# Performance work log

Hardware: AMD Instinct MI355X
Metric: run time of the kernel (lower is better)

Reference implementation:

```python
import jax, jax.numpy as jnp
import numpy as np
from jax import lax

B, C, H, W = 2, 64, 192, 192
KS = 3
N = KS * KS
L = 3  # num_gdns (ResBlocks)


def conv2d(x, w, b=None, padding=0):
    out = lax.conv_general_dilated(x, w, (1, 1), [(padding, padding)] * 2,
                                   dimension_numbers=('NCHW', 'OIHW', 'NCHW'))
    if b is not None:
        out = out + b[None, :, None, None]
    return out


def gdn(x, beta, gamma):
    # y = x / sqrt(beta + sum_j gamma_ij x_j^2)  (inverse=False)
    norm = conv2d(x * x, gamma[:, :, None, None], beta)
    return x / jnp.sqrt(norm)


def resblock(x, w1, w2, beta, gamma):
    res = x
    h = jax.nn.celu(gdn(conv2d(x, w1, padding=0), beta, gamma))  # conv1: no pad (H-2)
    return conv2d(h, w2, padding=2) + res  # conv2: pad 2 restores H


def deform_conv(x, offset, w_dc):
    # DCNv1 (pure-pytorch impl): offset (b,2N,h,w), rows first then cols.
    b, c, Hh, Ww = x.shape
    h, w = offset.shape[2], offset.shape[3]
    pad = 1
    xp = jnp.pad(x, ((0, 0), (0, 0), (pad, pad), (pad, pad)))
    Hp, Wp = Hh + 2 * pad, Ww + 2 * pad
    r = (KS - 1) // 2
    knr, knc = jnp.meshgrid(jnp.arange(-r, r + 1), jnp.arange(-r, r + 1), indexing='ij')
    p_n = jnp.concatenate([knr.reshape(-1), knc.reshape(-1)]).astype(x.dtype)  # (2N,)
    gr, gc = jnp.meshgrid(jnp.arange(1, h + 1), jnp.arange(1, w + 1), indexing='ij')
    p0 = jnp.concatenate([jnp.broadcast_to(gr[None], (N, h, w)),
                          jnp.broadcast_to(gc[None], (N, h, w))], 0).astype(x.dtype)  # (2N,h,w)
    p = p0[None] + p_n[None, :, None, None] + offset  # (b,2N,h,w)
    p = jnp.transpose(p, (0, 2, 3, 1))  # (b,h,w,2N)
    pr = jnp.clip(p[..., :N], 0, Hp - 1)
    pc = jnp.clip(p[..., N:], 0, Wp - 1)
    q0 = lax.stop_gradient(jnp.floor(p))
    qr0 = jnp.clip(q0[..., :N], 0, Hp - 1).astype(jnp.int32)
    qc0 = jnp.clip(q0[..., N:], 0, Wp - 1).astype(jnp.int32)
    qr1 = jnp.clip(q0[..., :N] + 1, 0, Hp - 1).astype(jnp.int32)
    qc1 = jnp.clip(q0[..., N:] + 1, 0, Wp - 1).astype(jnp.int32)
    # bilinear weights (match torch impl exactly)
    g_lt = (1 + (qr0 - pr)) * (1 + (qc0 - pc))
    g_rb = (1 - (qr1 - pr)) * (1 - (qc1 - pc))
    g_lb = (1 + (qr0 - pr)) * (1 - (qc1 - pc))
    g_rt = (1 - (qr1 - pr)) * (1 + (qc0 - pc))
    xf = xp.reshape(b, c, Hp * Wp)

    def gather(qr, qc):
        idx = (qr * Wp + qc).reshape(b, -1)  # (b, h*w*N)
        g = jax.vmap(lambda xb, ib: xb[:, ib])(xf, idx)  # (b,c,h*w*N)
        return g.reshape(b, c, h, w, N)

    xo = (g_lt[:, None] * gather(qr0, qc0) + g_rb[:, None] * gather(qr1, qc1)
          + g_lb[:, None] * gather(qr0, qc1) + g_rt[:, None] * gather(qr1, qc0))
    # stride-ks conv over reshaped x_offset == contraction over (c, n)
    wf = w_dc.reshape(w_dc.shape[0], c, N)
    return jnp.einsum('bchwn,ocn->bohw', xo, wf)


def setup_inputs() -> dict:
    key = jax.random.key(0)
    ks = jax.random.split(key, 11)
    f_r = jax.random.normal(ks[0], (B, C, H, W), jnp.float32)
    m_t = jax.random.normal(ks[1], (B, C, H, W), jnp.float32)
    w_pconv = jax.random.normal(ks[2], (2 * N, C, KS, KS), jnp.float32) * 0.01
    b_pconv = jax.random.normal(ks[3], (2 * N,), jnp.float32) * 0.01
    w_dc = jax.random.normal(ks[4], (C, C, KS, KS), jnp.float32) * 0.05
    w_cat = jax.random.normal(ks[5], (C, 2 * C, KS, KS), jnp.float32) * 0.05
    b_cat = jax.random.normal(ks[6], (C,), jnp.float32) * 0.05
    rb_w1 = jax.random.normal(ks[7], (L, C, C, KS, KS), jnp.float32) * 0.01
    rb_w2 = jax.random.normal(ks[8], (L, C, C, KS, KS), jnp.float32) * 0.01
    rb_beta = jax.random.uniform(ks[9], (L, C), jnp.float32) * 0.5 + 0.5
    rb_gamma = jnp.broadcast_to(0.1 * jnp.eye(C, dtype=jnp.float32), (L, C, C)) \
        + jax.random.uniform(ks[10], (L, C, C), jnp.float32) * 0.01
    return {"f_r": f_r, "m_t": m_t, "w_pconv": w_pconv, "b_pconv": b_pconv,
            "w_dc": w_dc, "w_cat": w_cat, "b_cat": b_cat,
            "rb_w1": rb_w1, "rb_w2": rb_w2, "rb_beta": rb_beta, "rb_gamma": rb_gamma}


def reference(f_r, m_t, w_pconv, b_pconv, w_dc, w_cat, b_cat, rb_w1, rb_w2, rb_beta, rb_gamma):
    offset = conv2d(m_t, w_pconv, b_pconv, padding=1)  # (B, 2N, H, W)
    x = deform_conv(f_r, offset, w_dc)                  # (B, C, H, W)
    y = conv2d(jnp.concatenate([x, f_r], axis=1), w_cat, b_cat, padding=1)
    for i in range(L):
        y = resblock(y, rb_w1[i], rb_w2[i], rb_beta[i], rb_gamma[i])
    return y + x
```

## Files before the change

kernel.cpp:

```cpp
#include <hip/hip_runtime.h>

typedef __attribute__((ext_vector_type(8))) __bf16 bf16x8;
typedef __attribute__((ext_vector_type(4))) __bf16 bf16x4;
typedef __attribute__((ext_vector_type(16))) float f32x16;
typedef __attribute__((ext_vector_type(4))) float f32x4;
typedef __attribute__((ext_vector_type(4))) int i32x4;

#define HH 192
#define WW 192
#define HW 36864
#define HW1 36100

#define TCS 144
#define RP66 (66 * TCS)
#define GDNPITCH 144
#define TREG 8704
#define TROW 5120
#define NPREP 1417

__device__ inline f32x16 mfma32(bf16x8 a, bf16x8 b, f32x16 c) {
  return __builtin_amdgcn_mfma_f32_32x32x16_bf16(a, b, c, 0, 0, 0);
}

__device__ inline f32x16 zero16() {
  f32x16 z;
#pragma unroll
  for (int e = 0; e < 16; ++e) z[e] = 0.f;
  return z;
}

__global__ __launch_bounds__(256) void prep_and_nhwc(
    const float* __restrict__ wp, const float* __restrict__ bp,
    const float* __restrict__ wdc, const float* __restrict__ wcat,
    const float* __restrict__ w1, const float* __restrict__ w2,
    const float* __restrict__ gamma,
    __bf16* __restrict__ wpA, __bf16* __restrict__ wdcA,
    __bf16* __restrict__ wcatA, __bf16* __restrict__ w1A,
    __bf16* __restrict__ w2A, __bf16* __restrict__ gA,
    float* __restrict__ bpad,
    const float* __restrict__ fr, const float* __restrict__ mt,
    __bf16* __restrict__ frn, __bf16* __restrict__ mtn) {
  __shared__ __align__(16) __bf16 tile[64 * 72];
  if (blockIdx.x >= NPREP) {
    int rem2 = blockIdx.x - NPREP;
    int tensor = rem2 / 1152, rem = rem2 % 1152;
    int b = rem / 576, p0 = (rem % 576) * 64;
    const float* src = (tensor ? mt : fr) + (size_t)b * 64 * HW;
    __bf16* dst = (tensor ? mtn : frn) + (size_t)b * HW * 64;
    int tid = threadIdx.x, c = tid >> 2, q0 = (tid & 3) * 16;
    const float* sp = src + (size_t)c * HW + p0 + q0;
#pragma unroll
    for (int qq = 0; qq < 4; ++qq) {
      f32x4 v = *(const f32x4*)(sp + qq * 4);
#pragma unroll
      for (int e = 0; e < 4; ++e) tile[(q0 + qq * 4 + e) * 72 + c] = (__bf16)v[e];
    }
    __syncthreads();
    int px = tid >> 2, c0 = (tid & 3) * 16;
    bf16x8 a = *(const bf16x8*)(&tile[px * 72 + c0]);
    bf16x8 b8 = *(const bf16x8*)(&tile[px * 72 + c0 + 8]);
    __bf16* dp = dst + (size_t)(p0 + px) * 64 + c0;
    *(bf16x8*)dp = a;
    *(bf16x8*)(dp + 8) = b8;
    return;
  }
  int i = blockIdx.x * 256 + threadIdx.x;
  if (i < 18432) {
    int j = i & 7, lane = (i >> 3) & 63, kc = (i >> 9) & 3, n = i >> 11;
    int o = lane & 31, c = kc * 16 + ((lane >> 5) << 3) + j;
    wpA[i] = (o < 18) ? (__bf16)wp[(o * 64 + c) * 9 + n] : (__bf16)0.f;
    return;
  }
  i -= 18432;
  if (i < 36864) {
    int j = i & 7, lane = (i >> 3) & 63, ot = (i >> 9) & 1, kc = (i >> 10) & 3, n = i >> 12;
    int o = ot * 32 + (lane & 31), c = kc * 16 + ((lane >> 5) << 3) + j;
    wdcA[i] = (__bf16)wdc[(o * 64 + c) * 9 + n];
    return;
  }
  i -= 36864;
  if (i < 73728) {
    int d = i, j = d & 7; d >>= 3; int lane = d & 63; d >>= 6; int ot = d & 1; d >>= 1;
    int kc = d & 7; int n = d >> 3;
    int o = ot * 32 + (lane & 31), c = kc * 16 + ((lane >> 5) << 3) + j;
    wcatA[i] = (__bf16)wcat[(o * 128 + c) * 9 + n];
    return;
  }
  i -= 73728;
  if (i < 110592) {
    int l = i / 36864, di = i % 36864, d = di;
    int j = d & 7; d >>= 3; int lane = d & 63; d >>= 6; int ot = d & 1; d >>= 1;
    int kc = d & 3; int n = d >> 2;
    int o = ot * 32 + (lane & 31), c = kc * 16 + ((lane >> 5) << 3) + j;
    w1A[l * 36864 + di] = (__bf16)w1[l * 36864 + (o * 64 + c) * 9 + n];
    return;
  }
  i -= 110592;
  if (i < 110592) {
    int l = i / 36864, di = i % 36864, d = di;
    int j = d & 7; d >>= 3; int lane = d & 63; d >>= 6; int ot = d & 1; d >>= 1;
    int kc = d & 3; int n = d >> 2;
    int o = ot * 32 + (lane & 31), c = kc * 16 + ((lane >> 5) << 3) + j;
    w2A[l * 36864 + di] = (__bf16)w2[l * 36864 + (o * 64 + c) * 9 + n];
    return;
  }
  i -= 110592;
  if (i < 12288) {
    int l = i / 4096, di = i % 4096, d = di;
    int j = d & 7; d >>= 3; int lane = d & 63; d >>= 6; int ot = d & 1; d >>= 1;
    int kc = d & 3;
    int o = ot * 32 + (lane & 31), c = kc * 16 + ((lane >> 5) << 3) + j;
    gA[l * 4096 + di] = (__bf16)gamma[l * 4096 + o * 64 + c];
    return;
  }
  i -= 12288;
  if (i < 96) bpad[i] = (i < 18) ? bp[i] : 0.f;
}

template <int ROWS, int COLS, int TPB>
__device__ inline void stage_bf16T(const __bf16* __restrict__ src,
                                   int srcH, int srcW, int row0, int col0,
                                   unsigned char* lds) {
  for (int i = threadIdx.x; i < ROWS * COLS * 8; i += TPB) {
    int r = i / (COLS * 8), rem = i - r * (COLS * 8), j = rem >> 3, u = rem & 7;
    int gr = row0 + r, gc = col0 + j;
    bf16x8 v;
#pragma unroll
    for (int e = 0; e < 8; ++e) v[e] = (__bf16)0.f;
    if (gr >= 0 && gr < srcH && gc >= 0 && gc < srcW)
      v = *(const bf16x8*)(src + ((size_t)gr * srcW + gc) * 64 + u * 8);
    *(bf16x8*)(lds + r * (COLS * TCS) + j * TCS + u * 16) = v;
  }
}

__device__ inline void stage_glds(const __bf16* __restrict__ src, int H, int W,
                                  int gr, int gc0, const __bf16* __restrict__ zpad,
                                  unsigned char* ldsrow, int chunk) {
  int l = threadIdx.x & 63;
  int colg = l >> 3, gsrc = (l & 7) ^ colg;
  int gc = gc0 + chunk * 8 + colg;
  const __bf16* gp = zpad;
  if (gr >= 0 && gr < H && gc >= 0 && gc < W)
    gp = src + ((size_t)gr * W + gc) * 64 + gsrc * 8;
  __builtin_amdgcn_global_load_lds(
      (const __attribute__((address_space(1))) void*)gp,
      (__attribute__((address_space(3))) void*)(ldsrow + chunk * 1024), 16, 0, 0);
}

template <int KCW>
__device__ inline void tapG1(const __bf16* __restrict__ aB, int ot, int pt,
                             const unsigned char* __restrict__ tile,
                             int n, int koff, f32x16& acc) {
  int lane = threadIdx.x & 63;
  int m = lane & 31, half = lane >> 5;
  int kh = n / 3, kw = n % 3;
  int p = kw + m, p7 = p & 7;
  bf16x8 A[4], B[4];
#pragma unroll
  for (int kc = 0; kc < 4; ++kc)
    A[kc] = *(const bf16x8*)(aB + (size_t)((n * KCW + koff + kc) * 2 + ot) * 512);
#pragma unroll
  for (int kc = 0; kc < 4; ++kc) {
    int gsl = ((kc * 2 + half) ^ p7) << 4;
    B[kc] = *(const bf16x8*)(tile + (kh + pt) * TROW + p * 128 + gsl);
  }
#pragma unroll
  for (int kc = 0; kc < 4; ++kc) acc = mfma32(A[kc], B[kc], acc);
}

__device__ inline void treg_write(const f32x16& a, int ot, unsigned char* reg) {
  int lane = threadIdx.x & 63;
  int m = lane & 31, half = lane >> 5;
#pragma unroll
  for (int g = 0; g < 4; ++g) {
    int o = ot * 32 + half * 4 + g * 8;
    f32x4 v;
    v[0] = a[g * 4 + 0]; v[1] = a[g * 4 + 1];
    v[2] = a[g * 4 + 2]; v[3] = a[g * 4 + 3];
    *(f32x4*)(reg + (m * 68 + o) * 4) = v;
  }
}

__device__ inline void merge_write(const f32x16 acc[2], unsigned char* mb) {
  int l = threadIdx.x & 63;
  unsigned char* p = mb + l * 128;
#pragma unroll
  for (int pt = 0; pt < 2; ++pt)
#pragma unroll
    for (int i = 0; i < 4; ++i) {
      f32x4 v;
      v[0] = acc[pt][i * 4 + 0]; v[1] = acc[pt][i * 4 + 1];
      v[2] = acc[pt][i * 4 + 2]; v[3] = acc[pt][i * 4 + 3];
      *(f32x4*)(p + (((pt * 4 + i) ^ (l & 7)) * 16)) = v;
    }
}
__device__ inline void merge_add(f32x16 acc[2], const unsigned char* mb) {
  int l = threadIdx.x & 63;
  const unsigned char* p = mb + l * 128;
#pragma unroll
  for (int pt = 0; pt < 2; ++pt)
#pragma unroll
    for (int i = 0; i < 4; ++i) {
      f32x4 v = *(const f32x4*)(p + (((pt * 4 + i) ^ (l & 7)) * 16));
      acc[pt][i * 4 + 0] += v[0]; acc[pt][i * 4 + 1] += v[1];
      acc[pt][i * 4 + 2] += v[2]; acc[pt][i * 4 + 3] += v[3];
    }
}

__device__ inline void acc32_to_lds(const f32x16 acc[2], unsigned char* reg) {
  int lane = threadIdx.x & 63;
  int colb = lane & 31, half = lane >> 5;
#pragma unroll
  for (int ot = 0; ot < 2; ++ot)
#pragma unroll
    for (int g = 0; g < 4; ++g) {
      int o = ot * 32 + half * 4 + g * 8;
      f32x4 v;
      v[0] = acc[ot][g * 4 + 0]; v[1] = acc[ot][g * 4 + 1];
      v[2] = acc[ot][g * 4 + 2]; v[3] = acc[ot][g * 4 + 3];
      *(f32x4*)(reg + (colb * 68 + o) * 4) = v;
    }
}

__global__ __launch_bounds__(256, 1) void pconv_mfma(
    const __bf16* __restrict__ mtn, const __bf16* __restrict__ wpA,
    const float* __restrict__ bpad, float* __restrict__ off20) {
  __shared__ __align__(16) unsigned char smem[6 * RP66];
  int b = blockIdx.x / 144, r = blockIdx.x % 144, rt = r / 3, ct = r % 3;
  int h0 = rt * 4, w0 = ct * 64;
  int wid = threadIdx.x >> 6, lane = threadIdx.x & 63;
  int colb = lane & 31, half = lane >> 5, kh8 = half << 3;
  stage_bf16T<6, 66, 256>(mtn + (size_t)b * HW * 64, 192, 192, h0 - 1, w0 - 1, smem);
  const __bf16* aB = wpA + lane * 8;
  bf16x8 pcur[4], pnxt[4];
#pragma unroll
  for (int kc = 0; kc < 4; ++kc) pcur[kc] = *(const bf16x8*)(aB + kc * 512);
  __syncthreads();
  f32x16 acc[2];
  acc[0] = zero16(); acc[1] = zero16();
  {
    const unsigned char* bB = smem + wid * RP66 + colb * TCS + kh8 * 2;
#pragma unroll
    for (int n = 0; n < 9; ++n) {
      if (n < 8) {
#pragma unroll
        for (int kc = 0; kc < 4; ++kc)
          pnxt[kc] = *(const bf16x8*)(aB + ((n + 1) * 4 + kc) * 512);
      }
      const int kh = n / 3, kw = n % 3;
#pragma unroll
      for (int kc = 0; kc < 4; ++kc) {
        const unsigned char* bp = bB + kh * RP66 + kw * TCS + kc * 32;
        bf16x8 b0 = *(const bf16x8*)(bp);
        bf16x8 b1 = *(const bf16x8*)(bp + 32 * TCS);
        acc[0] = mfma32(pcur[kc], b0, acc[0]);
        acc[1] = mfma32(pcur[kc], b1, acc[1]);
      }
#pragma unroll
      for (int kc = 0; kc < 4; ++kc) pcur[kc] = pnxt[kc];
    }
  }
  __syncthreads();
  unsigned char* reg = smem + wid * 9216;
#pragma unroll
  for (int pt = 0; pt < 2; ++pt)
#pragma unroll
    for (int g = 0; g < 4; ++g) {
      int o = half * 4 + g * 8;
      f32x4 v;
      v[0] = acc[pt][g * 4 + 0]; v[1] = acc[pt][g * 4 + 1];
      v[2] = acc[pt][g * 4 + 2]; v[3] = acc[pt][g * 4 + 3];
      *(f32x4*)(reg + ((pt * 32 + colb) * 36 + o) * 4) = v;
    }
  __builtin_amdgcn_s_waitcnt(0);
  size_t pix = (size_t)b * HW + (size_t)(h0 + wid) * 192 + w0 + lane;
#pragma unroll
  for (int q = 0; q < 5; ++q) {
    f32x4 v = *(const f32x4*)(reg + (lane * 36 + q * 4) * 4);
    v += *(const f32x4*)(bpad + q * 4);
    *(f32x4*)(off20 + pix * 20 + q * 4) = v;
  }
}

#define GOPITCH 32
#define DTBL (9 * 32 * GOPITCH)
#define DBUF 4608
#define DLDS (DTBL + 4 * DBUF)
__global__ __launch_bounds__(256, 2) void deform_mfma(
    const __bf16* __restrict__ frn, const float* __restrict__ off20,
    const __bf16* __restrict__ wdcA, float* __restrict__ xlow,
    __bf16* __restrict__ xlowb) {
  __shared__ __align__(16) unsigned char smem[DLDS];
  int bid = (blockIdx.x & 7) * 288 + (blockIdx.x >> 3);
  int b = bid / 1152, r = bid % 1152;
  int h = r / 6, s = r % 6;
  int w0 = s * 32;
  int tid = threadIdx.x;
  int wid = tid >> 6, lane = tid & 63;
  int m = lane & 31, half = lane >> 5;
  int pxg = lane >> 3, slot = lane & 7;
  const __bf16* xb = frn + (size_t)b * HW * 64;
  {
    int px = tid & 31, g = tid >> 5;
    int w = w0 + px;
    size_t pixl = (size_t)b * HW + (size_t)h * 192 + w;
    const float* ofp = off20 + pixl * 20;
    for (int n = g; n < 9; n += 8) {
      float offr = ofp[n], offc = ofp[9 + n];
      float pr = (float)(h + 1 + n / 3 - 1) + offr;
      float pc = (float)(w + 1 + n % 3 - 1) + offc;
      float prc = fminf(fmaxf(pr, 0.f), 193.f);
      float pcc = fminf(fmaxf(pc, 0.f), 193.f);
      float f0r = floorf(pr), f0c = floorf(pc);
      int qr0 = (int)fminf(fmaxf(f0r, 0.f), 193.f);
      int qc0 = (int)fminf(fmaxf(f0c, 0.f), 193.f);
      int qr1 = (int)fminf(fmaxf(f0r + 1.f, 0.f), 193.f);
      int qc1 = (int)fminf(fmaxf(f0c + 1.f, 0.f), 193.f);
      float dr0 = 1.f + ((float)qr0 - prc);
      float dr1 = 1.f - ((float)qr1 - prc);
      float dc0 = 1.f + ((float)qc0 - pcc);
      float dc1 = 1.f - ((float)qc1 - pcc);
      int o0, o1, o2, o3; float g0, g1, g2, g3;
      { bool v = (qr0 >= 1 && qr0 <= 192 && qc0 >= 1 && qc0 <= 192);
        o0 = min(max(qr0-1,0),191)*WW + min(max(qc0-1,0),191); g0 = v ? dr0*dc0 : 0.f; }
      { bool v = (qr1 >= 1 && qr1 <= 192 && qc1 >= 1 && qc1 <= 192);
        o1 = min(max(qr1-1,0),191)*WW + min(max(qc1-1,0),191); g1 = v ? dr1*dc1 : 0.f; }
      { bool v = (qr0 >= 1 && qr0 <= 192 && qc1 >= 1 && qc1 <= 192);
        o2 = min(max(qr0-1,0),191)*WW + min(max(qc1-1,0),191); g2 = v ? dr0*dc1 : 0.f; }
      { bool v = (qr1 >= 1 && qr1 <= 192 && qc0 >= 1 && qc0 <= 192);
        o3 = min(max(qr1-1,0),191)*WW + min(max(qc0-1,0),191); g3 = v ? dr1*dc0 : 0.f; }
      unsigned char* dst = smem + (n * 32 + px) * GOPITCH;
      f32x4 gv; gv[0] = g0; gv[1] = g1; gv[2] = g2; gv[3] = g3;
      i32x4 ov; ov[0] = o0; ov[1] = o1; ov[2] = o2; ov[3] = o3;
      *(f32x4*)dst = gv;
      *(i32x4*)(dst + 16) = ov;
    }
  }
  __syncthreads();
  f32x16 acc[2];
  acc[0] = zero16(); acc[1] = zero16();
  const __bf16* aB = wdcA + lane * 8;
  unsigned char* buf = smem + DTBL + wid * DBUF;
  const unsigned char* bB = buf + m * TCS + (half << 3) * 2;
  int n0 = (wid == 0) ? 0 : (wid * 2 + 1);
  int nn = (wid == 0) ? 3 : 2;

  bf16x8 C[4][4];
  f32x4 G[4];
  bf16x8 a[8];

  auto load_tap = [&](int n) {
#pragma unroll
    for (int i = 0; i < 4; ++i) {
      const unsigned char* gp = smem + (size_t)(n * 32 + i * 8 + pxg) * GOPITCH;
      i32x4 oi = *(const i32x4*)(gp + 16);
      G[i] = *(const f32x4*)gp;
#pragma unroll
      for (int j = 0; j < 4; ++j)
        C[i][j] = *(const bf16x8*)(xb + (size_t)oi[j] * 64 + slot * 8);
    }
  };
  auto load_a = [&](int n) {
#pragma unroll
    for (int kc = 0; kc < 4; ++kc) {
      a[kc * 2 + 0] = *(const bf16x8*)(aB + ((n * 4 + kc) * 2 + 0) * 512);
      a[kc * 2 + 1] = *(const bf16x8*)(aB + ((n * 4 + kc) * 2 + 1) * 512);
    }
  };
  auto blend_write = [&]() {
#pragma unroll
    for (int i = 0; i < 4; ++i) {
      bf16x8 ov;
#pragma unroll
      for (int e = 0; e < 8; ++e) {
        float f = G[i][0] * (float)C[i][0][e] + G[i][1] * (float)C[i][1][e] +
                  G[i][2] * (float)C[i][2][e] + G[i][3] * (float)C[i][3][e];
        ov[e] = (__bf16)f;
      }
      *(bf16x8*)(buf + (i * 8 + pxg) * TCS + slot * 16) = ov;
    }
  };
  auto consume = [&]() {
#pragma unroll
    for (int kc = 0; kc < 4; ++kc) {
      bf16x8 b0 = *(const bf16x8*)(bB + kc * 32);
      acc[0] = mfma32(a[kc * 2 + 0], b0, acc[0]);
      acc[1] = mfma32(a[kc * 2 + 1], b0, acc[1]);
    }
  };

  load_tap(n0);
  blend_write();
  for (int t = 1; t < nn; ++t) {
    load_a(n0 + t - 1);
    load_tap(n0 + t);
    consume();
    asm volatile("s_waitcnt lgkmcnt(0)" ::: "memory");
    blend_write();
  }
  load_a(n0 + nn - 1);
  consume();
  __syncthreads();
  if (wid) merge_write(acc, smem + (wid - 1) * 8192);
  __syncthreads();
  if (wid == 0) {
    merge_add(acc, smem);
    merge_add(acc, smem + 8192);
    merge_add(acc, smem + 16384);
    __builtin_amdgcn_s_waitcnt(0);
    unsigned char* reg = smem;
    acc32_to_lds(acc, reg);
    __builtin_amdgcn_s_waitcnt(0);
    int colb = m, ch = half * 32;
    size_t pix = (size_t)b * HW + (size_t)h * 192 + w0 + colb;
    float* dp = xlow + pix * 64 + ch;
    __bf16* dpb = xlowb + pix * 64 + ch;
#pragma unroll
    for (int q = 0; q < 8; ++q) {
      f32x4 v = *(const f32x4*)(reg + (colb * 68 + ch + q * 4) * 4);
      *(f32x4*)(dp + q * 4) = v;
      bf16x4 o8;
#pragma unroll
      for (int e = 0; e < 4; ++e) o8[e] = (__bf16)v[e];
      *(bf16x4*)(dpb + q * 4) = o8;
    }
  }
}

__global__ __launch_bounds__(256, 4) void convcat_mfma(
    const __bf16* __restrict__ xlowb, const __bf16* __restrict__ frn,
    const __bf16* __restrict__ wA, const float* __restrict__ bias,
    const __bf16* __restrict__ zpad, __bf16* __restrict__ y) {
  __shared__ __align__(16) unsigned char smem[2 * 4 * TROW];
  int bid = (blockIdx.x & 7) * 144 + (blockIdx.x >> 3);
  int b = bid / 576, r = bid % 576, rt = r / 6, ct = r % 6;
  int h0 = rt * 2, w0 = ct * 32;
  int tid = threadIdx.x, wid = tid >> 6, lane = tid & 63;
  int pt = wid & 1, ot = wid >> 1;
  int m = lane & 31, half = lane >> 5;
  const __bf16* src0 = xlowb + (size_t)b * HW * 64;
  const __bf16* src1 = frn + (size_t)b * HW * 64;
  for (int o = wid; o < 40; o += 4) {
    int t = o / 20, rr = (o % 20) / 5, ck = o % 5;
    stage_glds(t ? src1 : src0, 192, 192, h0 - 1 + rr, w0 - 1, zpad,
               smem + t * (4 * TROW) + rr * TROW, ck);
  }
  __syncthreads();
  const __bf16* aB = wA + lane * 8;
  f32x16 acc = zero16();
#pragma unroll
  for (int n = 0; n < 9; ++n) tapG1<8>(aB, ot, pt, smem, n, 0, acc);
#pragma unroll
  for (int n = 0; n < 9; ++n) tapG1<8>(aB, ot, pt, smem + 4 * TROW, n, 4, acc);
  __syncthreads();
  treg_write(acc, ot, smem + pt * TREG);
  __syncthreads();
  {
    const unsigned char* reg = smem + pt * TREG;
    int ch = ot * 32 + half * 16;
    int row = h0 + pt;
    __bf16* dp = y + ((size_t)b * HW + (size_t)row * 192 + w0 + m) * 64 + ch;
#pragma unroll
    for (int q = 0; q < 4; ++q) {
      f32x4 v = *(const f32x4*)(reg + (m * 68 + ch + q * 4) * 4);
      v += *(const f32x4*)(bias + ch + q * 4);
      bf16x4 o8;
#pragma unroll
      for (int e = 0; e < 4; ++e) o8[e] = (__bf16)v[e];
      *(bf16x4*)(dp + q * 4) = o8;
    }
  }
}

__global__ __launch_bounds__(256, 4) void conv1gdn_mfma(
    const __bf16* __restrict__ y, const __bf16* __restrict__ w1A,
    const __bf16* __restrict__ gA, const float* __restrict__ beta,
    const __bf16* __restrict__ zpad, __bf16* __restrict__ hbuf) {
  __shared__ __align__(16) unsigned char smem[9216 + 2 * TREG];
  int bid = (blockIdx.x & 7) * 144 + (blockIdx.x >> 3);
  int b = bid / 576, r = bid % 576, rt = r / 6, ct = r % 6;
  int h0 = rt * 2, w0 = ct * 32;
  int tid = threadIdx.x, wid = tid >> 6, lane = tid & 63;
  int pt = wid & 1, ot = wid >> 1;
  int m = lane & 31, half = lane >> 5, kh8 = half << 3;
  const __bf16* src = y + (size_t)b * HW * 64;
  for (int o = wid; o < 20; o += 4) {
    int rr = o / 5, ck = o % 5;
    stage_glds(src, 192, 192, h0 + rr, w0, zpad, smem + rr * TROW, ck);
  }
  __syncthreads();
  const __bf16* aB = w1A + lane * 8;
  f32x16 acc = zero16();
#pragma unroll
  for (int n = 0; n < 9; ++n) tapG1<4>(aB, ot, pt, smem, n, 0, acc);
  __syncthreads();
  unsigned char* gdnreg = smem;
  {
    int p = pt * 32 + m;
#pragma unroll
    for (int gg = 0; gg < 4; ++gg) {
      int o = ot * 32 + half * 4 + gg * 8;
      bf16x4 s;
#pragma unroll
      for (int e = 0; e < 4; ++e) {
        float x = acc[gg * 4 + e];
        s[e] = (__bf16)(x * x);
      }
      *(bf16x4*)(gdnreg + p * GDNPITCH + o * 2) = s;
    }
  }
  __syncthreads();
  {
    f32x16 nacc = zero16();
    const __bf16* gaB = gA + lane * 8;
    const unsigned char* gb = gdnreg + (pt * 32 + m) * GDNPITCH + kh8 * 2;
#pragma unroll
    for (int kc = 0; kc < 4; ++kc) {
      bf16x8 ga = *(const bf16x8*)(gaB + (kc * 2 + ot) * 512);
      bf16x8 b0 = *(const bf16x8*)(gb + kc * 32);
      nacc = mfma32(ga, b0, nacc);
    }
#pragma unroll
    for (int gg = 0; gg < 4; ++gg) {
      f32x4 bet = *(const f32x4*)(beta + ot * 32 + half * 4 + gg * 8);
#pragma unroll
      for (int e = 0; e < 4; ++e) {
        float nv = bet[e] + nacc[gg * 4 + e];
        float hv = acc[gg * 4 + e] * rsqrtf(nv);
        hv = hv > 0.f ? hv : expf(hv) - 1.f;
        acc[gg * 4 + e] = hv;
      }
    }
  }
  treg_write(acc, ot, smem + 9216 + pt * TREG);
  __syncthreads();
  {
    const unsigned char* reg = smem + 9216 + pt * TREG;
    int ch = ot * 32 + half * 16;
    int hr = h0 + pt, wcol = w0 + m;
    if (hr < 190 && wcol < 190) {
      __bf16* dp = hbuf + ((size_t)b * HW1 + (size_t)hr * 190 + wcol) * 64 + ch;
#pragma unroll
      for (int q = 0; q < 4; ++q) {
        f32x4 v = *(const f32x4*)(reg + (m * 68 + ch + q * 4) * 4);
        bf16x4 o8;
#pragma unroll
        for (int e = 0; e < 4; ++e) o8[e] = (__bf16)v[e];
        *(bf16x4*)(dp + q * 4) = o8;
      }
    }
  }
}

template <bool LAST>
__global__ __launch_bounds__(256, 4) void conv2_mfma(
    const __bf16* __restrict__ hbuf, const __bf16* __restrict__ w2A,
    const float* __restrict__ xlow, const __bf16* __restrict__ zpad,
    __bf16* __restrict__ y, float* __restrict__ out) {
  __shared__ __align__(16) unsigned char smem[4 * TROW];
  int bid = (blockIdx.x & 7) * 144 + (blockIdx.x >> 3);
  int b = bid / 576, r = bid % 576, rt = r / 6, ct = r % 6;
  int h0 = rt * 2, w0 = ct * 32;
  int tid = threadIdx.x, wid = tid >> 6, lane = tid & 63;
  int pt = wid & 1, ot = wid >> 1;
  int m = lane & 31, half = lane >> 5;
  const __bf16* src = hbuf + (size_t)b * HW1 * 64;
  for (int o = wid; o < 20; o += 4) {
    int rr = o / 5, ck = o % 5;
    stage_glds(src, 190, 190, h0 - 2 + rr, w0 - 2, zpad, smem + rr * TROW, ck);
  }
  __syncthreads();
  const __bf16* aB = w2A + lane * 8;
  f32x16 acc = zero16();
#pragma unroll
  for (int n = 0; n < 9; ++n) tapG1<4>(aB, ot, pt, smem, n, 0, acc);
  __syncthreads();
  treg_write(acc, ot, smem + pt * TREG);
  __syncthreads();
  {
    unsigned char* reg = smem + pt * TREG;
    int ch = ot * 32 + half * 16;
    int row = h0 + pt;
    size_t pix = (size_t)b * HW + (size_t)row * 192 + w0 + m;
    __bf16* yp = y + pix * 64 + ch;
    f32x4 v[4];
#pragma unroll
    for (int q = 0; q < 4; ++q) {
      v[q] = *(const f32x4*)(reg + (m * 68 + ch + q * 4) * 4);
      bf16x4 yv = *(const bf16x4*)(yp + q * 4);
#pragma unroll
      for (int e = 0; e < 4; ++e) v[q][e] += (float)yv[e];
    }
    if (!LAST) {
#pragma unroll
      for (int q = 0; q < 4; ++q) {
        bf16x4 o8;
#pragma unroll
        for (int e = 0; e < 4; ++e) o8[e] = (__bf16)v[q][e];
        *(bf16x4*)(yp + q * 4) = o8;
      }
    } else {
      const float* xp = xlow + pix * 64 + ch;
#pragma unroll
      for (int q = 0; q < 4; ++q) v[q] += *(const f32x4*)(xp + q * 4);
#pragma unroll
      for (int q = 0; q < 4; ++q)
        *(f32x4*)(reg + (m * 68 + ch + q * 4) * 4) = v[q];
      __syncthreads();
      int o = lane;
      float* op = out + ((size_t)b * 64 + o) * HW + (size_t)row * 192 + w0;
#pragma unroll
      for (int qq = 0; qq < 4; ++qq) {
        int q = ot * 4 + qq;
        f32x4 s;
#pragma unroll
        for (int e = 0; e < 4; ++e)
          s[e] = *(const float*)(reg + ((q * 4 + e) * 68 + o) * 4);
        *(f32x4*)(op + q * 4) = s;
      }
    }
  }
}

extern "C" void kernel_launch(void* const* d_in, const int* in_sizes, int n_in,
                              void* d_out, int out_size, void* d_ws, size_t ws_size,
                              hipStream_t stream) {
  const float* f_r      = (const float*)d_in[0];
  const float* m_t      = (const float*)d_in[1];
  const float* w_pconv  = (const float*)d_in[2];
  const float* b_pconv  = (const float*)d_in[3];
  const float* w_dc     = (const float*)d_in[4];
  const float* w_cat    = (const float*)d_in[5];
  const float* b_cat    = (const float*)d_in[6];
  const float* rb_w1    = (const float*)d_in[7];
  const float* rb_w2    = (const float*)d_in[8];
  const float* rb_beta  = (const float*)d_in[9];
  const float* rb_gamma = (const float*)d_in[10];
  float* out = (float*)d_out;

  float* ws = (float*)d_ws;
  float*  xlow  = ws;
  __bf16* ybuf  = (__bf16*)(xlow + 4718592);
  __bf16* xlowb = (__bf16*)(xlow + 4718592 + 2359296);
  float*  off20 = xlow + 4718592 + 4718592;
  __bf16* frn   = (__bf16*)(off20 + 1474560);
  __bf16* mtn   = (__bf16*)(off20 + 1474560 + 2359296);
  __bf16* hbuf  = mtn;
  float*  wbase = off20 + 1474560 + 2359296 + 2359296;
  __bf16* wpA   = (__bf16*)wbase;
  __bf16* wdcA  = (__bf16*)(wbase + 9216);
  __bf16* wcatA = (__bf16*)(wbase + 27648);
  __bf16* w1A   = (__bf16*)(wbase + 64512);
  __bf16* w2A   = (__bf16*)(wbase + 119808);
  __bf16* gA    = (__bf16*)(wbase + 175104);
  float*  bpad  = wbase + 181248;
  const __bf16* zpad = (const __bf16*)(bpad + 32);

  prep_and_nhwc<<<NPREP + 2304, 256, 0, stream>>>(
      w_pconv, b_pconv, w_dc, w_cat, rb_w1, rb_w2, rb_gamma,
      wpA, wdcA, wcatA, w1A, w2A, gA, bpad, f_r, m_t, frn, mtn);
  pconv_mfma<<<288, 256, 0, stream>>>(mtn, wpA, bpad, off20);
  deform_mfma<<<2304, 256, 0, stream>>>(frn, off20, wdcA, xlow, xlowb);
  convcat_mfma<<<1152, 256, 0, stream>>>(xlowb, frn, wcatA, b_cat, zpad, ybuf);
  for (int l = 0; l < 3; ++l) {
    conv1gdn_mfma<<<1152, 256, 0, stream>>>(ybuf, w1A + l * 36864, gA + l * 4096,
                                            rb_beta + l * 64, zpad, hbuf);
    if (l < 2)
      conv2_mfma<false><<<1152, 256, 0, stream>>>(hbuf, w2A + l * 36864, xlow, zpad, ybuf, out);
    else
      conv2_mfma<true><<<1152, 256, 0, stream>>>(hbuf, w2A + l * 36864, xlow, zpad, ybuf, out);
  }
}
```

Before: 258.0 us.

## Double-buffer two tiles per block in resblock convs to overlap loads with MFMA

The conv1+GDN and conv2 kernels now each handle two output tiles per block. The second tile's input is prefetched into a second LDS buffer via async global-to-LDS loads while the first tile is computed. The grid is halved and launch bounds drop from 4 to 3 blocks per CU to fit the doubled LDS. This hides load latency and trims the tail wave, at the cost of fewer resident blocks and less parallelism per launch.

```diff
diff --git a/kernel.cpp b/kernel.cpp
--- a/kernel.cpp
+++ b/kernel.cpp
@@ -16,6 +16,7 @@
 #define GDNPITCH 144
 #define TREG 8704
 #define TROW 5120
+#define TILE4 (4 * TROW)
 #define NPREP 1417
 
 __device__ inline f32x16 mfma32(bf16x8 a, bf16x8 b, f32x16 c) {
@@ -145,6 +146,17 @@
   __builtin_amdgcn_global_load_lds(
       (const __attribute__((address_space(1))) void*)gp,
       (__attribute__((address_space(3))) void*)(ldsrow + chunk * 1024), 16, 0, 0);
+}
+
+__device__ inline void stage_tile4(const __bf16* __restrict__ src, int H, int W,
+                                   int row0, int col0,
+                                   const __bf16* __restrict__ zpad,
+                                   unsigned char* buf) {
+  int wid = threadIdx.x >> 6;
+  for (int o = wid; o < 20; o += 4) {
+    int rr = o / 5, ck = o % 5;
+    stage_glds(src, H, W, row0 + rr, col0, zpad, buf + rr * TROW, ck);
+  }
 }
 
 template <int KCW>
@@ -431,7 +443,7 @@
     const __bf16* __restrict__ xlowb, const __bf16* __restrict__ frn,
     const __bf16* __restrict__ wA, const float* __restrict__ bias,
     const __bf16* __restrict__ zpad, __bf16* __restrict__ y) {
-  __shared__ __align__(16) unsigned char smem[2 * 4 * TROW];
+  __shared__ __align__(16) unsigned char smem[2 * TILE4];
   int bid = (blockIdx.x & 7) * 144 + (blockIdx.x >> 3);
   int b = bid / 576, r = bid % 576, rt = r / 6, ct = r % 6;
   int h0 = rt * 2, w0 = ct * 32;
@@ -443,7 +455,7 @@
   for (int o = wid; o < 40; o += 4) {
     int t = o / 20, rr = (o % 20) / 5, ck = o % 5;
     stage_glds(t ? src1 : src0, 192, 192, h0 - 1 + rr, w0 - 1, zpad,
-               smem + t * (4 * TROW) + rr * TROW, ck);
+               smem + t * TILE4 + rr * TROW, ck);
   }
   __syncthreads();
   const __bf16* aB = wA + lane * 8;
@@ -451,7 +463,7 @@
 #pragma unroll
   for (int n = 0; n < 9; ++n) tapG1<8>(aB, ot, pt, smem, n, 0, acc);
 #pragma unroll
-  for (int n = 0; n < 9; ++n) tapG1<8>(aB, ot, pt, smem + 4 * TROW, n, 4, acc);
+  for (int n = 0; n < 9; ++n) tapG1<8>(aB, ot, pt, smem + TILE4, n, 4, acc);
   __syncthreads();
   treg_write(acc, ot, smem + pt * TREG);
   __syncthreads();
@@ -472,29 +484,22 @@
   }
 }
 
-__global__ __launch_bounds__(256, 4) void conv1gdn_mfma(
-    const __bf16* __restrict__ y, const __bf16* __restrict__ w1A,
-    const __bf16* __restrict__ gA, const float* __restrict__ beta,
-    const __bf16* __restrict__ zpad, __bf16* __restrict__ hbuf) {
-  __shared__ __align__(16) unsigned char smem[9216 + 2 * TREG];
-  int bid = (blockIdx.x & 7) * 144 + (blockIdx.x >> 3);
-  int b = bid / 576, r = bid % 576, rt = r / 6, ct = r % 6;
+__device__ inline void conv1_tile(int t, const __bf16* __restrict__ w1A,
+                                  const __bf16* __restrict__ gA,
+                                  const float* __restrict__ beta,
+                                  __bf16* __restrict__ hbuf,
+                                  const unsigned char* __restrict__ buf,
+                                  unsigned char* __restrict__ work) {
+  int b = t / 576, r = t % 576, rt = r / 6, ct = r % 6;
   int h0 = rt * 2, w0 = ct * 32;
   int tid = threadIdx.x, wid = tid >> 6, lane = tid & 63;
   int pt = wid & 1, ot = wid >> 1;
   int m = lane & 31, half = lane >> 5, kh8 = half << 3;
-  const __bf16* src = y + (size_t)b * HW * 64;
-  for (int o = wid; o < 20; o += 4) {
-    int rr = o / 5, ck = o % 5;
-    stage_glds(src, 192, 192, h0 + rr, w0, zpad, smem + rr * TROW, ck);
-  }
-  __syncthreads();
   const __bf16* aB = w1A + lane * 8;
   f32x16 acc = zero16();
 #pragma unroll
-  for (int n = 0; n < 9; ++n) tapG1<4>(aB, ot, pt, smem, n, 0, acc);
-  __syncthreads();
-  unsigned char* gdnreg = smem;
+  for (int n = 0; n < 9; ++n) tapG1<4>(aB, ot, pt, buf, n, 0, acc);
+  __syncthreads();
   {
     int p = pt * 32 + m;
 #pragma unroll
@@ -506,14 +511,14 @@
         float x = acc[gg * 4 + e];
         s[e] = (__bf16)(x * x);
       }
-      *(bf16x4*)(gdnreg + p * GDNPITCH + o * 2) = s;
+      *(bf16x4*)(work + p * GDNPITCH + o * 2) = s;
     }
   }
   __syncthreads();
   {
     f32x16 nacc = zero16();
     const __bf16* gaB = gA + lane * 8;
-    const unsigned char* gb = gdnreg + (pt * 32 + m) * GDNPITCH + kh8 * 2;
+    const unsigned char* gb = work + (pt * 32 + m) * GDNPITCH + kh8 * 2;
 #pragma unroll
     for (int kc = 0; kc < 4; ++kc) {
       bf16x8 ga = *(const bf16x8*)(gaB + (kc * 2 + ot) * 512);
@@ -532,10 +537,11 @@
       }
     }
   }
-  treg_write(acc, ot, smem + 9216 + pt * TREG);
-  __syncthreads();
-  {
-    const unsigned char* reg = smem + 9216 + pt * TREG;
+  __syncthreads();
+  treg_write(acc, ot, work + pt * TREG);
+  __syncthreads();
+  {
+    const unsigned char* reg = work + pt * TREG;
     int ch = ot * 32 + half * 16;
     int hr = h0 + pt, wcol = w0 + m;
     if (hr < 190 && wcol < 190) {
@@ -552,33 +558,50 @@
   }
 }
 
+__global__ __launch_bounds__(256, 3) void conv1gdn_mfma(
+    const __bf16* __restrict__ y, const __bf16* __restrict__ w1A,
+    const __bf16* __restrict__ gA, const float* __restrict__ beta,
+    const __bf16* __restrict__ zpad, __bf16* __restrict__ hbuf) {
+  __shared__ __align__(16) unsigned char smem[2 * TILE4];
+  unsigned char* bufA = smem;
+  unsigned char* bufB = smem + TILE4;
+  int bid = (blockIdx.x & 7) * 72 + (blockIdx.x >> 3);
+  int t0 = bid, t1 = bid + 576;
+  {
+    int r = t0 % 576, rt = r / 6, ct = r % 6;
+    stage_tile4(y + (size_t)(t0 / 576) * HW * 64, 192, 192, rt * 2, ct * 32, zpad, bufA);
+  }
+  __syncthreads();
+  {
+    int r = t1 % 576, rt = r / 6, ct = r % 6;
+    stage_tile4(y + (size_t)(t1 / 576) * HW * 64, 192, 192, rt * 2, ct * 32, zpad, bufB);
+  }
+  conv1_tile(t0, w1A, gA, beta, hbuf, bufA, bufA);
+  __syncthreads();
+  conv1_tile(t1, w1A, gA, beta, hbuf, bufB, bufA);
+}
+
 template <bool LAST>
-__global__ __launch_bounds__(256, 4) void conv2_mfma(
-    const __bf16* __restrict__ hbuf, const __bf16* __restrict__ w2A,
-    const float* __restrict__ xlow, const __bf16* __restrict__ zpad,
-    __bf16* __restrict__ y, float* __restrict__ out) {
-  __shared__ __align__(16) unsigned char smem[4 * TROW];
-  int bid = (blockIdx.x & 7) * 144 + (blockIdx.x >> 3);
-  int b = bid / 576, r = bid % 576, rt = r / 6, ct = r % 6;
+__device__ inline void conv2_tile(int t, const __bf16* __restrict__ w2A,
+                                  const float* __restrict__ xlow,
+                                  __bf16* __restrict__ y,
+                                  float* __restrict__ out,
+                                  const unsigned char* __restrict__ buf,
+                                  unsigned char* __restrict__ work) {
+  int b = t / 576, r = t % 576, rt = r / 6, ct = r % 6;
   int h0 = rt * 2, w0 = ct * 32;
   int tid = threadIdx.x, wid = tid >> 6, lane = tid & 63;
   int pt = wid & 1, ot = wid >> 1;
   int m = lane & 31, half = lane >> 5;
-  const __bf16* src = hbuf + (size_t)b * HW1 * 64;
-  for (int o = wid; o < 20; o += 4) {
-    int rr = o / 5, ck = o % 5;
-    stage_glds(src, 190, 190, h0 - 2 + rr, w0 - 2, zpad, smem + rr * TROW, ck);
-  }
-  __syncthreads();
   const __bf16* aB = w2A + lane * 8;
   f32x16 acc = zero16();
 #pragma unroll
-  for (int n = 0; n < 9; ++n) tapG1<4>(aB, ot, pt, smem, n, 0, acc);
-  __syncthreads();
-  treg_write(acc, ot, smem + pt * TREG);
-  __syncthreads();
-  {
-    unsigned char* reg = smem + pt * TREG;
+  for (int n = 0; n < 9; ++n) tapG1<4>(aB, ot, pt, buf, n, 0, acc);
+  __syncthreads();
+  treg_write(acc, ot, work + pt * TREG);
+  __syncthreads();
+  {
+    unsigned char* reg = work + pt * TREG;
     int ch = ot * 32 + half * 16;
     int row = h0 + pt;
     size_t pix = (size_t)b * HW + (size_t)row * 192 + w0 + m;
@@ -620,6 +643,32 @@
       }
     }
   }
+}
+
+template <bool LAST>
+__global__ __launch_bounds__(256, 3) void conv2_mfma(
+    const __bf16* __restrict__ hbuf, const __bf16* __restrict__ w2A,
+    const float* __restrict__ xlow, const __bf16* __restrict__ zpad,
+    __bf16* __restrict__ y, float* __restrict__ out) {
+  __shared__ __align__(16) unsigned char smem[2 * TILE4];
+  unsigned char* bufA = smem;
+  unsigned char* bufB = smem + TILE4;
+  int bid = (blockIdx.x & 7) * 72 + (blockIdx.x >> 3);
+  int t0 = bid, t1 = bid + 576;
+  {
+    int r = t0 % 576, rt = r / 6, ct = r % 6;
+    stage_tile4(hbuf + (size_t)(t0 / 576) * HW1 * 64, 190, 190,
+                rt * 2 - 2, ct * 32 - 2, zpad, bufA);
+  }
+  __syncthreads();
+  {
+    int r = t1 % 576, rt = r / 6, ct = r % 6;
+    stage_tile4(hbuf + (size_t)(t1 / 576) * HW1 * 64, 190, 190,
+                rt * 2 - 2, ct * 32 - 2, zpad, bufB);
+  }
+  conv2_tile<LAST>(t0, w2A, xlow, y, out, bufA, bufA);
+  __syncthreads();
+  conv2_tile<LAST>(t1, w2A, xlow, y, out, bufB, bufA);
 }
 
 extern "C" void kernel_launch(void* const* d_in, const int* in_sizes, int n_in,
@@ -663,11 +712,11 @@
   deform_mfma<<<2304, 256, 0, stream>>>(frn, off20, wdcA, xlow, xlowb);
   convcat_mfma<<<1152, 256, 0, stream>>>(xlowb, frn, wcatA, b_cat, zpad, ybuf);
   for (int l = 0; l < 3; ++l) {
-    conv1gdn_mfma<<<1152, 256, 0, stream>>>(ybuf, w1A + l * 36864, gA + l * 4096,
-                                            rb_beta + l * 64, zpad, hbuf);
+    conv1gdn_mfma<<<576, 256, 0, stream>>>(ybuf, w1A + l * 36864, gA + l * 4096,
+                                           rb_beta + l * 64, zpad, hbuf);
     if (l < 2)
-      conv2_mfma<false><<<1152, 256, 0, stream>>>(hbuf, w2A + l * 36864, xlow, zpad, ybuf, out);
+      conv2_mfma<false><<<576, 256, 0, stream>>>(hbuf, w2A + l * 36864, xlow, zpad, ybuf, out);
     else
-      conv2_mfma<true><<<1152, 256, 0, stream>>>(hbuf, w2A + l * 36864, xlow, zpad, ybuf, out);
-  }
-}
+      conv2_mfma<true><<<576, 256, 0, stream>>>(hbuf, w2A + l * 36864, xlow, zpad, ybuf, out);
+  }
+}
```

Measured after the change: 262.8 us. About the same (+1.8%).
